# Kernel optimization log

Hardware: AMD Instinct MI355X
Metric: run time of the kernel (lower is better)

## Reference

```python
import jax, jax.numpy as jnp
import numpy as np

N_NODES = 50000
N_EDGES = 800000
IN_CH, HID_CH, OUT_CH = 128, 256, 128


def _glorot(key, shape):
    fan_in, fan_out = shape[1], shape[0]
    lim = float(np.sqrt(6.0 / (fan_in + fan_out)))
    return jax.random.uniform(key, shape, jnp.float32, -lim, lim)


def setup_inputs() -> dict:
    key = jax.random.key(0)
    ks = jax.random.split(key, 8)
    x = jax.random.normal(ks[0], (N_NODES, IN_CH), jnp.float32)
    edge_index = jax.random.randint(ks[1], (2, N_EDGES), 0, N_NODES, jnp.int64)
    return {
        "x": x,
        "edge_index": edge_index,
        # layer 1: SAGEConv(128 -> 256): lin_l (with bias) on aggregated, lin_r (no bias) on root
        "W1l": _glorot(ks[2], (HID_CH, IN_CH)),
        "b1l": jnp.zeros((HID_CH,), jnp.float32),
        "W1r": _glorot(ks[3], (HID_CH, IN_CH)),
        # layer 2: SAGEConv(256 -> 128)
        "W2l": _glorot(ks[4], (OUT_CH, HID_CH)),
        "b2l": jnp.zeros((OUT_CH,), jnp.float32),
        "W2r": _glorot(ks[5], (OUT_CH, HID_CH)),
    }


def _sage_conv(x, src, dst, Wl, bl, Wr, n_nodes):
    # mean-aggregate neighbor (source) features at destination nodes
    msg = x[src]                                                   # [E, C] gather
    agg = jax.ops.segment_sum(msg, dst, num_segments=n_nodes)      # [N, C]
    deg = jax.ops.segment_sum(jnp.ones((src.shape[0],), x.dtype), dst,
                              num_segments=n_nodes)                # [N]
    mean = agg / jnp.maximum(deg, 1.0)[:, None]                    # zero-degree -> 0
    return mean @ Wl.T + bl + x @ Wr.T


def reference(x, edge_index, W1l, b1l, W1r, W2l, b2l, W2r):
    src, dst = edge_index[0], edge_index[1]
    n = x.shape[0]
    h = _sage_conv(x, src, dst, W1l, b1l, W1r, n)
    h = jax.nn.relu(h)  # dropout is identity in eval mode
    out = _sage_conv(h, src, dst, W2l, b2l, W2r, n)
    return out
```

## Files before the change

### kernel.cpp

```cpp
#include <hip/hip_runtime.h>

#define N_NODES 50000
#define IN_CH   128
#define HID_CH  256
#define OUT_CH  128

#define NB    196
#define NWG   64
#define NBNW  (NB * NWG)
#define SCHUNK 49

#define XBLK  3125
#define WBLK  64

typedef __attribute__((ext_vector_type(8))) short bf16x8;
typedef __attribute__((ext_vector_type(4))) float f32x4;

__device__ __forceinline__ unsigned short f32_bf16_rne(float f) {
    unsigned u = __float_as_uint(f);
    unsigned r = u + 0x7fff + ((u >> 16) & 1);
    return (unsigned short)(r >> 16);
}
__device__ __forceinline__ float bf16lo_f32(unsigned u) { return __uint_as_float(u << 16); }
__device__ __forceinline__ float bf16hi_f32(unsigned u) { return __uint_as_float(u & 0xffff0000u); }

__device__ __forceinline__ void cvt8(const float* __restrict__ in,
                                     unsigned short* __restrict__ outp, size_t j)
{
    const float4* p = reinterpret_cast<const float4*>(in) + 2 * j;
    float4 a = p[0], b = p[1];
    alignas(16) unsigned short t[8] = {
        f32_bf16_rne(a.x), f32_bf16_rne(a.y), f32_bf16_rne(a.z), f32_bf16_rne(a.w),
        f32_bf16_rne(b.x), f32_bf16_rne(b.y), f32_bf16_rne(b.z), f32_bf16_rne(b.w)};
    *reinterpret_cast<int4*>(outp + 8 * j) = *reinterpret_cast<const int4*>(t);
}

__global__ __launch_bounds__(256) void prep_kernel(
    const int* __restrict__ src, const int* __restrict__ dst,
    int* __restrict__ counts, int E, int chunk,
    const float* __restrict__ x, unsigned short* __restrict__ xb,
    const float* __restrict__ W1l, const float* __restrict__ W1r,
    const float* __restrict__ W2l, const float* __restrict__ W2r,
    unsigned short* __restrict__ W1lb, unsigned short* __restrict__ W1rb,
    unsigned short* __restrict__ W2lb, unsigned short* __restrict__ W2rb)
{
    const int b = blockIdx.x;
    if (b < NWG) {
        __shared__ int h[NB];
        for (int i = threadIdx.x; i < NB; i += 256) h[i] = 0;
        __syncthreads();
        const int e0 = b * chunk;
        const int e1 = min(e0 + chunk, E);
        for (int e = e0 + threadIdx.x; e < e1; e += 256) {
            int s = src[e], d = dst[e];
            if ((unsigned)s < (unsigned)N_NODES && (unsigned)d < (unsigned)N_NODES)
                atomicAdd(&h[d >> 8], 1);
        }
        __syncthreads();
        for (int i = threadIdx.x; i < NB; i += 256)
            counts[i * NWG + b] = h[i];
    } else if (b < NWG + XBLK) {
        size_t j = (size_t)(b - NWG) * 256 + threadIdx.x;
        cvt8(x, xb, j);
    } else {
        int idx = (b - NWG - XBLK) * 256 + threadIdx.x;
        int seg = idx >> 12, j = idx & 4095;
        const float* in = (seg == 0) ? W1l : (seg == 1) ? W1r : (seg == 2) ? W2l : W2r;
        unsigned short* o = (seg == 0) ? W1lb : (seg == 1) ? W1rb : (seg == 2) ? W2lb : W2rb;
        cvt8(in, o, (size_t)j);
    }
}

__global__ __launch_bounds__(256) void scan_all_kernel(
    const int* __restrict__ counts, int* __restrict__ S)
{
    __shared__ int tot[256];
    const int t = threadIdx.x;
    const int base = t * SCHUNK;
    int loc[SCHUNK];
    int sum = 0;
#pragma unroll
    for (int k = 0; k < SCHUNK; ++k) {
        loc[k] = sum;
        sum += counts[base + k];
    }
    tot[t] = sum;
    __syncthreads();
    for (int off = 1; off < 256; off <<= 1) {
        int v = (t >= off) ? tot[t - off] : 0;
        __syncthreads();
        if (t >= off) tot[t] += v;
        __syncthreads();
    }
    int offv = (t == 0) ? 0 : tot[t - 1];
#pragma unroll
    for (int k = 0; k < SCHUNK; ++k)
        S[base + k] = loc[k] + offv;
    if (t == 255) S[NBNW] = offv + sum;
}

__global__ __launch_bounds__(256) void bscatter_kernel(
    const int* __restrict__ src, const int* __restrict__ dst,
    const int* __restrict__ S, int* __restrict__ pairs, int E, int chunk)
{
    __shared__ int cur[NB];
    const int w = blockIdx.x;
    for (int i = threadIdx.x; i < NB; i += 256) cur[i] = S[i * NWG + w];
    __syncthreads();
    const int e0 = w * chunk;
    const int e1 = min(e0 + chunk, E);
    for (int e = e0 + threadIdx.x; e < e1; e += 256) {
        int s = src[e], d = dst[e];
        if ((unsigned)s < (unsigned)N_NODES && (unsigned)d < (unsigned)N_NODES) {
            int pos = atomicAdd(&cur[d >> 8], 1);
            pairs[pos] = (s << 8) | (d & 255);
        }
    }
}

__global__ __launch_bounds__(256) void bsort_kernel(
    const int* __restrict__ pairs, const int* __restrict__ S,
    int* __restrict__ rowptr, int* __restrict__ colidx)
{
    __shared__ int hcnt[256];
    __shared__ int hcur[256];
    const int b = blockIdx.x;
    const int start = S[b * NWG];
    const int endv  = (b == NB - 1) ? S[NBNW] : S[(b + 1) * NWG];

    hcnt[threadIdx.x] = 0;
    __syncthreads();
    for (int e = start + threadIdx.x; e < endv; e += 256)
        atomicAdd(&hcnt[pairs[e] & 255], 1);
    __syncthreads();
    for (int off = 1; off < 256; off <<= 1) {
        int t = (threadIdx.x >= off) ? hcnt[threadIdx.x - off] : 0;
        __syncthreads();
        if (threadIdx.x >= off) hcnt[threadIdx.x] += t;
        __syncthreads();
    }
    int offv = (threadIdx.x == 0) ? 0 : hcnt[threadIdx.x - 1];
    hcur[threadIdx.x] = offv;
    int node = (b << 8) + threadIdx.x;
    if (node < N_NODES) rowptr[node] = start + offv;
    if (b == NB - 1 && threadIdx.x == 0) rowptr[N_NODES] = endv;
    __syncthreads();
    for (int e = start + threadIdx.x; e < endv; e += 256) {
        int p = pairs[e];
        int pos = atomicAdd(&hcur[p & 255], 1);
        colidx[start + pos] = (unsigned)p >> 8;
    }
}

#define ACCUM_ROW(v)                                            \
    acc[0] += bf16lo_f32(v.x); acc[1] += bf16hi_f32(v.x);       \
    acc[2] += bf16lo_f32(v.y); acc[3] += bf16hi_f32(v.y);       \
    acc[4] += bf16lo_f32(v.z); acc[5] += bf16hi_f32(v.z);       \
    acc[6] += bf16lo_f32(v.w); acc[7] += bf16hi_f32(v.w);

#define AGG_BODY(CH)                                                            \
    const int node = blockIdx.x * 4 + (threadIdx.x >> 6);                       \
    if (node >= N_NODES) return;                                                \
    const int lane = threadIdx.x & 63;                                          \
    const int grp = lane >> 4, ch = lane & 15;                                  \
    const int beg = rowptr[node], end = rowptr[node + 1];                       \
    const int len = end - beg;                                                  \
    const int q = (len + 3) >> 2;                                               \
    int j  = beg + grp * q;                                                     \
    int j1 = min(j + q, end);                                                   \
    float acc[8] = {};                                                          \
    for (; j + 3 < j1; j += 4) {                                                \
        int s0 = colidx[j],     s1 = colidx[j + 1];                             \
        int s2 = colidx[j + 2], s3 = colidx[j + 3];                             \
        int4 v0 = *reinterpret_cast<const int4*>(feat + (size_t)s0 * CH + ch * 8); \
        int4 v1 = *reinterpret_cast<const int4*>(feat + (size_t)s1 * CH + ch * 8); \
        int4 v2 = *reinterpret_cast<const int4*>(feat + (size_t)s2 * CH + ch * 8); \
        int4 v3 = *reinterpret_cast<const int4*>(feat + (size_t)s3 * CH + ch * 8); \
        ACCUM_ROW(v0) ACCUM_ROW(v1) ACCUM_ROW(v2) ACCUM_ROW(v3)                 \
    }                                                                           \
    for (; j < j1; ++j) {                                                       \
        int s0 = colidx[j];                                                     \
        int4 v0 = *reinterpret_cast<const int4*>(feat + (size_t)s0 * CH + ch * 8); \
        ACCUM_ROW(v0)                                                           \
    }                                                                           \
    _Pragma("unroll")                                                           \
    for (int k = 0; k < 8; ++k) {                                               \
        acc[k] += __shfl_xor(acc[k], 16);                                       \
        acc[k] += __shfl_xor(acc[k], 32);                                       \
    }                                                                           \
    const float sc = 1.0f / fmaxf((float)len, 1.0f);

__global__ __launch_bounds__(256) void agg1_kernel(
    const unsigned short* __restrict__ feat, const int* __restrict__ rowptr,
    const int* __restrict__ colidx, unsigned short* __restrict__ outp)
{
    AGG_BODY(IN_CH)
    if (grp == 0) {
        alignas(16) unsigned short t[8];
#pragma unroll
        for (int k = 0; k < 8; ++k) t[k] = f32_bf16_rne(acc[k] * sc);
        *reinterpret_cast<int4*>(outp + (size_t)node * IN_CH + ch * 8) =
            *reinterpret_cast<const int4*>(t);
    }
}

__global__ __launch_bounds__(256) void agg2_kernel(
    const unsigned short* __restrict__ feat, const int* __restrict__ rowptr,
    const int* __restrict__ colidx, float* __restrict__ out)
{
    AGG_BODY(OUT_CH)
    if (grp == 0) {
        float* o = out + (size_t)node * OUT_CH + ch * 8;
        float4 o0 = reinterpret_cast<float4*>(o)[0];
        float4 o1 = reinterpret_cast<float4*>(o)[1];
        o0.x += acc[0] * sc; o0.y += acc[1] * sc; o0.z += acc[2] * sc; o0.w += acc[3] * sc;
        o1.x += acc[4] * sc; o1.y += acc[5] * sc; o1.z += acc[6] * sc; o1.w += acc[7] * sc;
        reinterpret_cast<float4*>(o)[0] = o0;
        reinterpret_cast<float4*>(o)[1] = o1;
    }
}

__device__ __forceinline__ void stage_async(
    const unsigned short* __restrict__ g, int ldg, int rowBase, int maxRow,
    int kBase, unsigned short* __restrict__ s, int tid)
{
    const int wave = tid >> 6;
    const int lane = tid & 63;
    const int r_in = lane >> 3;
    const int c_g  = (lane & 7) ^ r_in;
#pragma unroll
    for (int it = 0; it < 4; ++it) {
        const int rowBlk = it * 32 + wave * 8;
        int row = rowBase + rowBlk + r_in;
        if (row >= maxRow) row = maxRow - 1;
        const unsigned short* gp = g + (size_t)row * ldg + kBase + c_g * 8;
        unsigned short* lp = s + rowBlk * 64;
        __builtin_amdgcn_global_load_lds(
            (const __attribute__((address_space(1))) unsigned int*)gp,
            (__attribute__((address_space(3))) unsigned int*)lp,
            16, 0, 0);
    }
}

__device__ __forceinline__ const bf16x8* frag_ptr(
    const unsigned short* __restrict__ s, int rr, int c)
{
    return reinterpret_cast<const bf16x8*>(s + rr * 64 + (((c ^ (rr & 7))) << 3));
}

__device__ __forceinline__ void mfma_tile(
    const unsigned short* __restrict__ As, const unsigned short* __restrict__ Bs,
    int wm, int wn, int l16, int quad, f32x4 acc[4][4])
{
#pragma unroll
    for (int k0 = 0; k0 < 64; k0 += 32) {
        const int c = (k0 >> 3) + quad;
        bf16x8 a[4], b[4];
#pragma unroll
        for (int i = 0; i < 4; ++i)
            a[i] = *frag_ptr(As, wm * 64 + i * 16 + l16, c);
#pragma unroll
        for (int j = 0; j < 4; ++j)
            b[j] = *frag_ptr(Bs, wn * 64 + j * 16 + l16, c);
#pragma unroll
        for (int i = 0; i < 4; ++i)
#pragma unroll
            for (int j = 0; j < 4; ++j)
                acc[i][j] = __builtin_amdgcn_mfma_f32_16x16x32_bf16(
                    b[j], a[i], acc[i][j], 0, 0, 0);
    }
}

__global__ __launch_bounds__(256) void gemm1_mfma(
    const unsigned short* __restrict__ mean1b, const unsigned short* __restrict__ xb,
    const unsigned short* __restrict__ W1lb,   const unsigned short* __restrict__ W1rb,
    const float* __restrict__ b1l, unsigned short* __restrict__ hb)
{
    __shared__ unsigned short As[128 * 64];
    __shared__ unsigned short Bs[128 * 64];
    const int tid = threadIdx.x;
    const int wid = tid >> 6, lane = tid & 63;
    const int wm = wid & 1, wn = wid >> 1;
    const int l16 = lane & 15, quad = lane >> 4;
    const int rowBase = blockIdx.x * 128;
    const int colBase = blockIdx.y * 128;

    f32x4 z = {0.f, 0.f, 0.f, 0.f};
    f32x4 acc[4][4];
#pragma unroll
    for (int i = 0; i < 4; ++i)
#pragma unroll
        for (int j = 0; j < 4; ++j) acc[i][j] = z;

#pragma unroll
    for (int op = 0; op < 2; ++op) {
        const unsigned short* A = op ? xb : mean1b;
        const unsigned short* B = op ? W1rb : W1lb;
#pragma unroll
        for (int kb = 0; kb < IN_CH; kb += 64) {
            __syncthreads();
            stage_async(A, IN_CH, rowBase, N_NODES, kb, As, tid);
            stage_async(B, IN_CH, colBase, HID_CH, kb, Bs, tid);
            __syncthreads();
            mfma_tile(As, Bs, wm, wn, l16, quad, acc);
        }
    }

#pragma unroll
    for (int i = 0; i < 4; ++i) {
        int m = rowBase + wm * 64 + i * 16 + l16;
        if (m >= N_NODES) continue;
#pragma unroll
        for (int j = 0; j < 4; ++j) {
            int col = colBase + wn * 64 + j * 16 + quad * 4;
            float4 bv = *reinterpret_cast<const float4*>(b1l + col);
            alignas(8) unsigned short t[4];
            t[0] = f32_bf16_rne(fmaxf(acc[i][j][0] + bv.x, 0.0f));
            t[1] = f32_bf16_rne(fmaxf(acc[i][j][1] + bv.y, 0.0f));
            t[2] = f32_bf16_rne(fmaxf(acc[i][j][2] + bv.z, 0.0f));
            t[3] = f32_bf16_rne(fmaxf(acc[i][j][3] + bv.w, 0.0f));
            *reinterpret_cast<uint2*>(hb + (size_t)m * HID_CH + col) =
                *reinterpret_cast<const uint2*>(t);
        }
    }
}

__global__ __launch_bounds__(256) void gemm2_mfma(
    const unsigned short* __restrict__ hb, const unsigned short* __restrict__ W2lb,
    const unsigned short* __restrict__ W2rb, const float* __restrict__ b2l,
    unsigned short* __restrict__ pb, float* __restrict__ out)
{
    __shared__ unsigned short As[128 * 64];
    __shared__ unsigned short Bs[128 * 64];
    const int tid = threadIdx.x;
    const int wid = tid >> 6, lane = tid & 63;
    const int wm = wid & 1, wn = wid >> 1;
    const int l16 = lane & 15, quad = lane >> 4;
    const int rowBase = blockIdx.x * 128;
    const unsigned short* B = blockIdx.y ? W2rb : W2lb;

    f32x4 z = {0.f, 0.f, 0.f, 0.f};
    f32x4 acc[4][4];
#pragma unroll
    for (int i = 0; i < 4; ++i)
#pragma unroll
        for (int j = 0; j < 4; ++j) acc[i][j] = z;

#pragma unroll
    for (int kb = 0; kb < HID_CH; kb += 64) {
        __syncthreads();
        stage_async(hb, HID_CH, rowBase, N_NODES, kb, As, tid);
        stage_async(B, HID_CH, 0, OUT_CH, kb, Bs, tid);
        __syncthreads();
        mfma_tile(As, Bs, wm, wn, l16, quad, acc);
    }

    if (blockIdx.y == 0) {
#pragma unroll
        for (int i = 0; i < 4; ++i) {
            int m = rowBase + wm * 64 + i * 16 + l16;
            if (m >= N_NODES) continue;
#pragma unroll
            for (int j = 0; j < 4; ++j) {
                int col = wn * 64 + j * 16 + quad * 4;
                alignas(8) unsigned short t[4];
                t[0] = f32_bf16_rne(acc[i][j][0]);
                t[1] = f32_bf16_rne(acc[i][j][1]);
                t[2] = f32_bf16_rne(acc[i][j][2]);
                t[3] = f32_bf16_rne(acc[i][j][3]);
                *reinterpret_cast<uint2*>(pb + (size_t)m * OUT_CH + col) =
                    *reinterpret_cast<const uint2*>(t);
            }
        }
    } else {
#pragma unroll
        for (int i = 0; i < 4; ++i) {
            int m = rowBase + wm * 64 + i * 16 + l16;
            if (m >= N_NODES) continue;
#pragma unroll
            for (int j = 0; j < 4; ++j) {
                int col = wn * 64 + j * 16 + quad * 4;
                float4 bv = *reinterpret_cast<const float4*>(b2l + col);
                float4 o;
                o.x = acc[i][j][0] + bv.x;
                o.y = acc[i][j][1] + bv.y;
                o.z = acc[i][j][2] + bv.z;
                o.w = acc[i][j][3] + bv.w;
                *reinterpret_cast<float4*>(out + (size_t)m * OUT_CH + col) = o;
            }
        }
    }
}

extern "C" void kernel_launch(void* const* d_in, const int* in_sizes, int n_in,
                              void* d_out, int out_size, void* d_ws, size_t ws_size,
                              hipStream_t stream)
{
    const float* x   = (const float*)d_in[0];
    const int*   ei  = (const int*)d_in[1];
    const float* W1l = (const float*)d_in[2];
    const float* b1l = (const float*)d_in[3];
    const float* W1r = (const float*)d_in[4];
    const float* W2l = (const float*)d_in[5];
    const float* b2l = (const float*)d_in[6];
    const float* W2r = (const float*)d_in[7];

    const int E = in_sizes[1] / 2;
    const int* src = ei;
    const int* dst = ei + E;

    char* ws = (char*)d_ws;
    size_t off = 0;
    auto alloc = [&](size_t bytes) {
        void* p = ws + off;
        off += (bytes + 255) & ~(size_t)255;
        return p;
    };
    unsigned short* xb     = (unsigned short*)alloc((size_t)N_NODES * IN_CH * 2);
    unsigned short* mean1b = (unsigned short*)alloc((size_t)N_NODES * IN_CH * 2);
    unsigned short* hb     = (unsigned short*)alloc((size_t)N_NODES * HID_CH * 2);
    unsigned short* pb     = (unsigned short*)alloc((size_t)N_NODES * OUT_CH * 2);
    unsigned short* W1lb   = (unsigned short*)alloc((size_t)HID_CH * IN_CH * 2);
    unsigned short* W1rb   = (unsigned short*)alloc((size_t)HID_CH * IN_CH * 2);
    unsigned short* W2lb   = (unsigned short*)alloc((size_t)OUT_CH * HID_CH * 2);
    unsigned short* W2rb   = (unsigned short*)alloc((size_t)OUT_CH * HID_CH * 2);
    int* counts = (int*)alloc((size_t)NBNW * 4);
    int* S      = (int*)alloc((size_t)(NBNW + 1) * 4);
    int* pairs  = (int*)alloc((size_t)E * 4);
    int* rowptr = (int*)alloc((size_t)(N_NODES + 1) * 4);
    int* colidx = (int*)alloc((size_t)E * 4);
    float* out = (float*)d_out;

    const int chunk = (E + NWG - 1) / NWG;

    prep_kernel<<<NWG + XBLK + WBLK, 256, 0, stream>>>(
        src, dst, counts, E, chunk, x, xb,
        W1l, W1r, W2l, W2r, W1lb, W1rb, W2lb, W2rb);
    scan_all_kernel<<<1, 256, 0, stream>>>(counts, S);
    bscatter_kernel<<<NWG, 256, 0, stream>>>(src, dst, S, pairs, E, chunk);
    bsort_kernel<<<NB, 256, 0, stream>>>(pairs, S, rowptr, colidx);

    const int aggBlocks = (N_NODES + 3) / 4;
    const int mBlocks = (N_NODES + 127) / 128;

    agg1_kernel<<<aggBlocks, 256, 0, stream>>>(xb, rowptr, colidx, mean1b);
    gemm1_mfma<<<dim3(mBlocks, HID_CH / 128), 256, 0, stream>>>(
        mean1b, xb, W1lb, W1rb, b1l, hb);
    gemm2_mfma<<<dim3(mBlocks, 2), 256, 0, stream>>>(hb, W2lb, W2rb, b2l, pb, out);
    agg2_kernel<<<aggBlocks, 256, 0, stream>>>(pb, rowptr, colidx, out);
}
```

Measured before the change: 242.8 us.

## Split aggregation channels across grid.y and spread edges over eight lane groups

The mean-aggregation kernels now split the 128 feature channels into four 32-channel slices handled by blockIdx.y. Each wave uses eight edge groups of eight lanes, each lane loading 4 bf16 values (8 bytes) instead of 16 bytes per row. This raises parallelism per node and the number of independent gathers, but each source row is now fetched by four separate blocks in 64-byte pieces. The colidx/rowptr reads are repeated four times, and the gathers are less coalesced.

```diff
diff --git a/kernel.cpp b/kernel.cpp
--- a/kernel.cpp
+++ b/kernel.cpp
@@ -152,39 +152,36 @@
     }
 }
 
-#define ACCUM_ROW(v)                                            \
+#define ACC4(v)                                                 \
     acc[0] += bf16lo_f32(v.x); acc[1] += bf16hi_f32(v.x);       \
-    acc[2] += bf16lo_f32(v.y); acc[3] += bf16hi_f32(v.y);       \
-    acc[4] += bf16lo_f32(v.z); acc[5] += bf16hi_f32(v.z);       \
-    acc[6] += bf16lo_f32(v.w); acc[7] += bf16hi_f32(v.w);
+    acc[2] += bf16lo_f32(v.y); acc[3] += bf16hi_f32(v.y);
 
 #define AGG_BODY(CH)                                                            \
     const int node = blockIdx.x * 4 + (threadIdx.x >> 6);                       \
     if (node >= N_NODES) return;                                                \
     const int lane = threadIdx.x & 63;                                          \
-    const int grp = lane >> 4, ch = lane & 15;                                  \
+    const int grp = lane >> 3;                                        \
+    const int chOff = blockIdx.y * 32 + (lane & 7) * 4;                         \
     const int beg = rowptr[node], end = rowptr[node + 1];                       \
     const int len = end - beg;                                                  \
-    const int q = (len + 3) >> 2;                                               \
+    const int q = (len + 7) >> 3;                                               \
     int j  = beg + grp * q;                                                     \
     int j1 = min(j + q, end);                                                   \
-    float acc[8] = {};                                                          \
-    for (; j + 3 < j1; j += 4) {                                                \
-        int s0 = colidx[j],     s1 = colidx[j + 1];                             \
-        int s2 = colidx[j + 2], s3 = colidx[j + 3];                             \
-        int4 v0 = *reinterpret_cast<const int4*>(feat + (size_t)s0 * CH + ch * 8); \
-        int4 v1 = *reinterpret_cast<const int4*>(feat + (size_t)s1 * CH + ch * 8); \
-        int4 v2 = *reinterpret_cast<const int4*>(feat + (size_t)s2 * CH + ch * 8); \
-        int4 v3 = *reinterpret_cast<const int4*>(feat + (size_t)s3 * CH + ch * 8); \
-        ACCUM_ROW(v0) ACCUM_ROW(v1) ACCUM_ROW(v2) ACCUM_ROW(v3)                 \
+    float acc[4] = {};                                                          \
+    for (; j + 1 < j1; j += 2) {                                                \
+        int s0 = colidx[j], s1 = colidx[j + 1];                                 \
+        int2 v0 = *reinterpret_cast<const int2*>(feat + (size_t)s0 * CH + chOff); \
+        int2 v1 = *reinterpret_cast<const int2*>(feat + (size_t)s1 * CH + chOff); \
+        ACC4(v0) ACC4(v1)                                                       \
     }                                                                           \
-    for (; j < j1; ++j) {                                                       \
+    if (j < j1) {                                                               \
         int s0 = colidx[j];                                                     \
-        int4 v0 = *reinterpret_cast<const int4*>(feat + (size_t)s0 * CH + ch * 8); \
-        ACCUM_ROW(v0)                                                           \
+        int2 v0 = *reinterpret_cast<const int2*>(feat + (size_t)s0 * CH + chOff); \
+        ACC4(v0)                                                                \
     }                                                                           \
     _Pragma("unroll")                                                           \
-    for (int k = 0; k < 8; ++k) {                                               \
+    for (int k = 0; k < 4; ++k) {                                               \
+        acc[k] += __shfl_xor(acc[k], 8);                                        \
         acc[k] += __shfl_xor(acc[k], 16);                                       \
         acc[k] += __shfl_xor(acc[k], 32);                                       \
     }                                                                           \
@@ -196,11 +193,11 @@
 {
     AGG_BODY(IN_CH)
     if (grp == 0) {
-        alignas(16) unsigned short t[8];
-#pragma unroll
-        for (int k = 0; k < 8; ++k) t[k] = f32_bf16_rne(acc[k] * sc);
-        *reinterpret_cast<int4*>(outp + (size_t)node * IN_CH + ch * 8) =
-            *reinterpret_cast<const int4*>(t);
+        alignas(8) unsigned short t[4];
+#pragma unroll
+        for (int k = 0; k < 4; ++k) t[k] = f32_bf16_rne(acc[k] * sc);
+        *reinterpret_cast<int2*>(outp + (size_t)node * IN_CH + chOff) =
+            *reinterpret_cast<const int2*>(t);
     }
 }
 
@@ -210,13 +207,11 @@
 {
     AGG_BODY(OUT_CH)
     if (grp == 0) {
-        float* o = out + (size_t)node * OUT_CH + ch * 8;
-        float4 o0 = reinterpret_cast<float4*>(o)[0];
-        float4 o1 = reinterpret_cast<float4*>(o)[1];
-        o0.x += acc[0] * sc; o0.y += acc[1] * sc; o0.z += acc[2] * sc; o0.w += acc[3] * sc;
-        o1.x += acc[4] * sc; o1.y += acc[5] * sc; o1.z += acc[6] * sc; o1.w += acc[7] * sc;
-        reinterpret_cast<float4*>(o)[0] = o0;
-        reinterpret_cast<float4*>(o)[1] = o1;
+        float* o = out + (size_t)node * OUT_CH + chOff;
+        float4 ov = *reinterpret_cast<float4*>(o);
+        ov.x += acc[0] * sc; ov.y += acc[1] * sc;
+        ov.z += acc[2] * sc; ov.w += acc[3] * sc;
+        *reinterpret_cast<float4*>(o) = ov;
     }
 }
 
@@ -443,9 +438,9 @@
     const int aggBlocks = (N_NODES + 3) / 4;
     const int mBlocks = (N_NODES + 127) / 128;
 
-    agg1_kernel<<<aggBlocks, 256, 0, stream>>>(xb, rowptr, colidx, mean1b);
+    agg1_kernel<<<dim3(aggBlocks, 4), 256, 0, stream>>>(xb, rowptr, colidx, mean1b);
     gemm1_mfma<<<dim3(mBlocks, HID_CH / 128), 256, 0, stream>>>(
         mean1b, xb, W1lb, W1rb, b1l, hb);
     gemm2_mfma<<<dim3(mBlocks, 2), 256, 0, stream>>>(hb, W2lb, W2rb, b2l, pb, out);
-    agg2_kernel<<<aggBlocks, 256, 0, stream>>>(pb, rowptr, colidx, out);
-}
+    agg2_kernel<<<dim3(aggBlocks, 4), 256, 0, stream>>>(pb, rowptr, colidx, out);
+}
```

Result: slower. 309.9 us (+27.6%).
